# Kernel optimization log

Hardware: AMD Instinct MI355X
Metric: run time of the kernel (lower is better)

Reference implementation:

```python
import jax, jax.numpy as jnp
import numpy as np

B, N, K = 8, 12500, 64           # graphs, nodes/graph, sort-pool k
E_PER = 200000                   # edges per graph (avg degree 16)
TOTAL_N = B * N
TOTAL_E = B * E_PER
NEG_SLOPE = 0.01
EPS = 1e-5


def setup_inputs() -> dict:
    key = jax.random.key(0)
    ks = jax.random.split(key, 8)
    # per-graph local edge endpoints, then offset into the global node index space
    offs = (jnp.arange(B, dtype=jnp.int32) * N)[:, None]
    src = (jax.random.randint(ks[0], (B, E_PER), 0, N, dtype=jnp.int32) + offs).reshape(-1)
    dst = (jax.random.randint(ks[1], (B, E_PER), 0, N, dtype=jnp.int32) + offs).reshape(-1)
    return {
        "features": jax.random.normal(ks[2], (TOTAL_N, 64), dtype=jnp.float32),
        "edge_weights": jax.random.uniform(ks[3], (TOTAL_E,), dtype=jnp.float32),
        "W1": jax.random.normal(ks[4], (64, 128), dtype=jnp.float32) * (1.0 / np.sqrt(64)),
        "W2": jax.random.normal(ks[5], (128, 32), dtype=jnp.float32) * (1.0 / np.sqrt(128)),
        "gamma1": jnp.ones((128,), jnp.float32),
        "beta1": jnp.zeros((128,), jnp.float32),
        "alpha1": jnp.ones((128,), jnp.float32),
        "gamma2": jnp.ones((32,), jnp.float32),
        "beta2": jnp.zeros((32,), jnp.float32),
        "alpha2": jnp.ones((32,), jnp.float32),
        "edge_src": src,
        "edge_dst": dst,
    }


def _leaky(x):
    return jnp.where(x >= 0, x, NEG_SLOPE * x)


def _graph_conv(feat, W, src, dst, ew):
    # DGL GraphConv, norm='both', bias=False, with edge_weight.
    ones = jnp.ones((TOTAL_E,), feat.dtype)
    out_deg = jnp.maximum(jax.ops.segment_sum(ones, src, num_segments=TOTAL_N), 1.0)
    in_deg = jnp.maximum(jax.ops.segment_sum(ones, dst, num_segments=TOTAL_N), 1.0)
    h = (feat * jax.lax.rsqrt(out_deg)[:, None]) @ W          # project (linear, order-invariant)
    msg = h[src] * ew[:, None]                                 # [E, out]
    agg = jax.ops.segment_sum(msg, dst, num_segments=TOTAL_N)  # SpMM scatter
    return agg * jax.lax.rsqrt(in_deg)[:, None]


def _graph_norm(feat, gamma, beta, alpha):
    # per-graph GraphNorm: (x - alpha*mean) / sqrt(var(x - alpha*mean) + eps) * gamma + beta
    x = feat.reshape(B, N, -1)
    mean = x.mean(axis=1, keepdims=True)
    sub = x - alpha * mean
    var = (sub * sub).mean(axis=1, keepdims=True)
    out = gamma * sub * jax.lax.rsqrt(var + EPS) + beta
    return out.reshape(TOTAL_N, -1)


def _sort_pool(feat):
    # DGL SortPooling: sort each node's features ascending, take top-K nodes by last channel.
    x = jnp.sort(feat.reshape(B, N, -1), axis=-1)
    _, idx = jax.lax.top_k(x[..., -1], K)                      # [B, K], descending
    sel = jnp.take_along_axis(x, idx[..., None], axis=1)       # [B, K, D]
    return sel.reshape(B, -1)


def reference(features, edge_weights, W1, W2, gamma1, beta1, alpha1,
              gamma2, beta2, alpha2, edge_src, edge_dst):
    h1 = _graph_conv(features, W1, edge_src, edge_dst, edge_weights)
    h1 = _leaky(_graph_norm(h1, gamma1, beta1, alpha1))
    r1 = _sort_pool(h1)                                        # [B, K*128]
    h2 = _graph_conv(h1, W2, edge_src, edge_dst, edge_weights)
    h2 = _leaky(_graph_norm(h2, gamma2, beta2, alpha2))
    r2 = _sort_pool(h2)                                        # [B, K*32]
    return _leaky(jnp.concatenate([r1, r2], axis=1))           # [B, K*(128+32)]
```

## Files before the change

### kernel.cpp

```cpp
#include <hip/hip_runtime.h>
#include <cstdint>

constexpr int B_       = 8;
constexpr int NPG_     = 12500;
constexpr int KSEL_    = 64;
constexpr int TOTAL_N_ = 100000;
constexpr int TOTAL_E_ = 1600000;
constexpr int EPG_     = 200000;
constexpr int NKEY_    = 16384;
constexpr int OUT_ROW  = KSEL_ * (128 + 32);
constexpr int NB_SCAN  = (TOTAL_N_ + 255) / 256;
constexpr int BPG_     = (EPG_ + 255) / 256;

constexpr int TROWS_   = 32;
constexpr int NT_DST   = 391;
constexpr int NT_SRC   = 4;
constexpr int SRC_TW   = 3125;
constexpr int LBKT_    = NT_DST * 8 * NT_SRC;
constexpr int NBKT     = B_ * LBKT_;
constexpr int NB_BSCAN = NBKT / 256;

constexpr int BLKG_    = 16;
constexpr int NHB_     = B_ * BLKG_;
constexpr int ESLICE_  = EPG_ / BLKG_;

typedef float f2v __attribute__((ext_vector_type(2)));
typedef int   i2v __attribute__((ext_vector_type(2)));

__device__ __forceinline__ float lrelu(float v){ return v >= 0.f ? v : 0.01f * v; }
__device__ __forceinline__ int   rlanei(int x, int l){ return __builtin_amdgcn_readlane(x, l); }
__device__ __forceinline__ float rlanef(float x, int l){
  return __uint_as_float(__builtin_amdgcn_readlane((int)__float_as_uint(x), l));
}

__device__ __forceinline__ void edge_key(int s, int d, int& key, int& pk){
  int g   = d / NPG_;
  int dlc = d - g * NPG_;
  int slc = s - g * NPG_;
  int dt  = dlc >> 5;
  int dl  = dlc & 31;
  int w   = dl >> 2;
  int st  = slc / SRC_TW;
  key = (((g * NT_DST + dt) * 8 + w) * NT_SRC) + st;
  pk  = (slc << 2) | (dl & 3);
}

__global__ __launch_bounds__(1024, 1)
void hist_priv(const int* __restrict__ src, const int* __restrict__ dst,
               int* __restrict__ out_part,
               int* __restrict__ bkt_part,
               unsigned short* __restrict__ lrank){
  __shared__ int oh[NPG_];
  __shared__ int bh[LBKT_];
  int t  = threadIdx.x;
  int hb = blockIdx.x;
  int g  = hb & 7, sb = hb >> 3;
  for (int i = t; i < NPG_;  i += 1024) oh[i] = 0;
  for (int i = t; i < LBKT_; i += 1024) bh[i] = 0;
  __syncthreads();
  int ebase = g * EPG_ + sb * ESLICE_;
  for (int i = t; i < ESLICE_; i += 1024){
    int e = ebase + i;
    int s = src[e], d = dst[e];
    atomicAdd(&oh[s - g * NPG_], 1);
    int key, pk; edge_key(s, d, key, pk);
    int r = atomicAdd(&bh[key - g * LBKT_], 1);
    lrank[e] = (unsigned short)r;
  }
  __syncthreads();
  int* op = out_part + (size_t)hb * NPG_;
  int* bp = bkt_part + (size_t)hb * LBKT_;
  for (int i = t; i < NPG_;  i += 1024) op[i] = oh[i];
  for (int i = t; i < LBKT_; i += 1024) bp[i] = bh[i];
}

__global__ void hist_reduce_nodes(const int* __restrict__ out_part, float* __restrict__ rsq_out){
  int i = blockIdx.x * 256 + threadIdx.x;
  if (i < TOTAL_N_){
    int g = i / NPG_, nl = i - g * NPG_;
    int s = 0;
    #pragma unroll
    for (int sb = 0; sb < BLKG_; ++sb) s += out_part[(size_t)(sb * 8 + g) * NPG_ + nl];
    if (s < 1) s = 1;
    rsq_out[i] = rsqrtf((float)s);
  }
}

__global__ void hist_reduce_bkt(int* __restrict__ bkt_part, int* __restrict__ bcnt){
  int k = blockIdx.x * 256 + threadIdx.x;
  if (k < NBKT){
    int g = k / LBKT_, lk = k - g * LBKT_;
    int run = 0;
    #pragma unroll
    for (int sb = 0; sb < BLKG_; ++sb){
      size_t idx = (size_t)(sb * 8 + g) * LBKT_ + lk;
      int v = bkt_part[idx];
      bkt_part[idx] = run;
      run += v;
    }
    bcnt[k] = run;
  }
}

__global__ void scan_blocks(const int* __restrict__ cnt, int* __restrict__ off,
                            int* __restrict__ bsum, int n){
  __shared__ int tmp[256];
  int t = threadIdx.x;
  int i = blockIdx.x * 256 + t;
  int x = (i < n) ? cnt[i] : 0;
  tmp[t] = x;
  __syncthreads();
  for (int d = 1; d < 256; d <<= 1){
    int v = (t >= d) ? tmp[t - d] : 0;
    __syncthreads();
    tmp[t] += v;
    __syncthreads();
  }
  if (i < n) off[i] = tmp[t] - x;
  if (t == 255) bsum[blockIdx.x] = tmp[255];
}

__global__ void scan_sums(int* __restrict__ bsum, int nb){
  __shared__ int tmp[512];
  int t = threadIdx.x;
  int x = (t < nb) ? bsum[t] : 0;
  tmp[t] = x;
  __syncthreads();
  for (int d = 1; d < 512; d <<= 1){
    int v = (t >= d) ? tmp[t - d] : 0;
    __syncthreads();
    tmp[t] += v;
    __syncthreads();
  }
  if (t < nb) bsum[t] = tmp[t] - x;
}

__global__ void scan_add(int* __restrict__ off, const int* __restrict__ bsum, int n){
  int i = blockIdx.x * 256 + threadIdx.x;
  if (i < n) off[i] += bsum[blockIdx.x];
}

__global__ void bfill2(const int* __restrict__ src, const int* __restrict__ dst,
                       const float* __restrict__ ew, const float* __restrict__ rsq_out,
                       const unsigned short* __restrict__ lrank,
                       const int* __restrict__ bkt_part, const int* __restrict__ boff,
                       i2v* __restrict__ bkt){
  int g  = blockIdx.x & 7;
  int il = (blockIdx.x >> 3) * 256 + threadIdx.x;
  if (il < EPG_){
    int e = g * EPG_ + il;
    int s = src[e], d = dst[e];
    int key, pk; edge_key(s, d, key, pk);
    int lk = key - g * LBKT_;
    int sb = il / ESLICE_;
    int slot = boff[key] + bkt_part[(size_t)(sb * 8 + g) * LBKT_ + lk] + (int)lrank[e];
    i2v v; v.x = pk; v.y = __float_as_int(ew[e] * rsq_out[s]);
    bkt[slot] = v;
  }
}

__global__ __launch_bounds__(512, 4)
void spmm1_tile(const int* __restrict__ boff, const i2v* __restrict__ bkt,
                const float* __restrict__ feat, const float* __restrict__ W1,
                float* __restrict__ rsq_in, float* __restrict__ h1,
                float* __restrict__ gsum, float* __restrict__ gsq){
  __shared__ float wsh[64 * 128];
  __shared__ float sred[4][512];
  int t = threadIdx.x;
  int w = t >> 6, lane = t & 63;
  int g = blockIdx.x & 7, dt = blockIdx.x >> 3;

  for (int i = t; i < 64 * 128; i += 512) wsh[i] = W1[i];

  int kbase = (((g * NT_DST + dt) * 8) + w) * NT_SRC;
  int e0 = boff[kbase];
  int e1 = (kbase + NT_SRC < NBKT) ? boff[kbase + NT_SRC] : TOTAL_E_;

  const float* fg = feat + (size_t)g * NPG_ * 64;
  float a0 = 0.f, a1 = 0.f, a2 = 0.f, a3 = 0.f;
  int cntp = 0;

#define ACC1(P, Q, F) { int r_ = (P) & 3; float q_ = (Q);                 \
    a0 = fmaf((r_ == 0) ? q_ : 0.f, (F), a0);                             \
    a1 = fmaf((r_ == 1) ? q_ : 0.f, (F), a1);                             \
    a2 = fmaf((r_ == 2) ? q_ : 0.f, (F), a2);                             \
    a3 = fmaf((r_ == 3) ? q_ : 0.f, (F), a3);                             \
    cntp += 1 << (r_ << 3); }

  #pragma unroll 1
  for (int e = e0; e < e1; e += 64){
    int m = e1 - e; if (m > 64) m = 64;
    int pk = 0; float wr = 0.f;
    if (lane < m){ i2v ed = bkt[e + lane]; pk = ed.x; wr = __int_as_float(ed.y); }
    int j = 0;
    #pragma unroll 1
    for (; j + 8 <= m; j += 8){
      int   p0 = rlanei(pk, j+0), p1 = rlanei(pk, j+1), p2 = rlanei(pk, j+2), p3 = rlanei(pk, j+3);
      int   p4 = rlanei(pk, j+4), p5 = rlanei(pk, j+5), p6 = rlanei(pk, j+6), p7 = rlanei(pk, j+7);
      float q0 = rlanef(wr, j+0), q1 = rlanef(wr, j+1), q2 = rlanef(wr, j+2), q3 = rlanef(wr, j+3);
      float q4 = rlanef(wr, j+4), q5 = rlanef(wr, j+5), q6 = rlanef(wr, j+6), q7 = rlanef(wr, j+7);
      float f0 = fg[(size_t)(p0 >> 2) * 64 + lane];
      float f1 = fg[(size_t)(p1 >> 2) * 64 + lane];
      float f2 = fg[(size_t)(p2 >> 2) * 64 + lane];
      float f3 = fg[(size_t)(p3 >> 2) * 64 + lane];
      float f4 = fg[(size_t)(p4 >> 2) * 64 + lane];
      float f5 = fg[(size_t)(p5 >> 2) * 64 + lane];
      float f6 = fg[(size_t)(p6 >> 2) * 64 + lane];
      float f7 = fg[(size_t)(p7 >> 2) * 64 + lane];
      ACC1(p0, q0, f0); ACC1(p1, q1, f1); ACC1(p2, q2, f2); ACC1(p3, q3, f3);
      ACC1(p4, q4, f4); ACC1(p5, q5, f5); ACC1(p6, q6, f6); ACC1(p7, q7, f7);
    }
    #pragma unroll 1
    for (; j < m; ++j){
      int   p = rlanei(pk, j);
      float q = rlanef(wr, j);
      float f = fg[(size_t)(p >> 2) * 64 + lane];
      ACC1(p, q, f);
    }
  }
#undef ACC1

  __syncthreads();

  int rows = NPG_ - dt * TROWS_; if (rows > TROWS_) rows = TROWS_;
  const f2v* wp = (const f2v*)wsh;
  f2v A0 = {0.f,0.f}, A1 = {0.f,0.f}, A2 = {0.f,0.f}, A3 = {0.f,0.f};
  #pragma unroll 1
  for (int k = 0; k < 64; ++k){
    f2v wv = wp[k * 64 + lane];
    float b0 = rlanef(a0, k), b1 = rlanef(a1, k), b2 = rlanef(a2, k), b3 = rlanef(a3, k);
    A0.x = fmaf(b0, wv.x, A0.x); A0.y = fmaf(b0, wv.y, A0.y);
    A1.x = fmaf(b1, wv.x, A1.x); A1.y = fmaf(b1, wv.y, A1.y);
    A2.x = fmaf(b2, wv.x, A2.x); A2.y = fmaf(b2, wv.y, A2.y);
    A3.x = fmaf(b3, wv.x, A3.x); A3.y = fmaf(b3, wv.y, A3.y);
  }
  float s0 = 0.f, q0 = 0.f, s1 = 0.f, q1 = 0.f;
  #pragma unroll
  for (int r = 0; r < 4; ++r){
    int lr = w * 4 + r;
    if (lr < rows){
      f2v A = (r == 0) ? A0 : (r == 1) ? A1 : (r == 2) ? A2 : A3;
      int cr = (cntp >> (r << 3)) & 255;
      float ri = rsqrtf((float)(cr < 1 ? 1 : cr));
      int node = g * NPG_ + dt * TROWS_ + lr;
      if (lane == 0) rsq_in[node] = ri;
      A.x *= ri; A.y *= ri;
      __builtin_nontemporal_store(A, (f2v*)&h1[(size_t)node * 128 + 2 * lane]);
      s0 += A.x; q0 = fmaf(A.x, A.x, q0);
      s1 += A.y; q1 = fmaf(A.y, A.y, q1);
    }
  }
  __syncthreads();
  sred[0][t] = s0; sred[1][t] = q0; sred[2][t] = s1; sred[3][t] = q1;
  __syncthreads();
  if (t < 64){
    float S0 = 0.f, Q0 = 0.f, S1 = 0.f, Q1 = 0.f;
    #pragma unroll
    for (int ww = 0; ww < 8; ++ww){
      S0 += sred[0][t + 64*ww]; Q0 += sred[1][t + 64*ww];
      S1 += sred[2][t + 64*ww]; Q1 += sred[3][t + 64*ww];
    }
    atomicAdd(&gsum[g * 128 + 2*t],     S0);
    atomicAdd(&gsq [g * 128 + 2*t],     Q0);
    atomicAdd(&gsum[g * 128 + 2*t + 1], S1);
    atomicAdd(&gsq [g * 128 + 2*t + 1], Q1);
  }
}

__global__ void finalize1(const float* __restrict__ gsum, const float* __restrict__ gsq,
                          const float* __restrict__ gamma, const float* __restrict__ beta,
                          const float* __restrict__ alpha, float* __restrict__ mul, float* __restrict__ add){
  int i = threadIdx.x;
  int c = i & 127;
  const float invn = 1.0f / (float)NPG_;
  float m = gsum[i] * invn;
  float a = alpha[c];
  float var = gsq[i] * invn - 2.f * a * m * m + a * a * m * m;
  float mu = gamma[c] * rsqrtf(var + 1e-5f);
  mul[i] = mu;
  add[i] = beta[c] - mu * a * m;
}

__global__ __launch_bounds__(256, 4)
void normproj(const float* __restrict__ h1,
              const float* __restrict__ mul, const float* __restrict__ add,
              const float* __restrict__ W2,
              unsigned long long* __restrict__ keys, float* __restrict__ h2p){
  __shared__ float w2s[128 * 32];
  int t = threadIdx.x;
  for (int i = t; i < 128 * 32; i += 256) w2s[i] = W2[i];
  __syncthreads();

  int g     = blockIdx.x & 7;
  int wslot = (blockIdx.x >> 3) * 4 + (t >> 6);
  int lane  = t & 63;
  int c     = lane & 31, hh = lane >> 5;
  int wbase = hh * 64 * 32 + c;

  float m0 = mul[g * 128 + lane],      aa0 = add[g * 128 + lane];
  float m1 = mul[g * 128 + 64 + lane], aa1 = add[g * 128 + 64 + lane];

  int nv = (NPG_ - wslot + 511) / 512;

  int v0 = g * NPG_ + wslot;
  float x0 = __builtin_nontemporal_load(&h1[(size_t)v0 * 128 + lane]);
  float x1 = __builtin_nontemporal_load(&h1[(size_t)v0 * 128 + 64 + lane]);

  for (int i = 0; i < nv; ++i){
    int v = g * NPG_ + wslot + i * 512;
    float cur0 = x0, cur1 = x1;
    if (i + 1 < nv){
      int vn = v + 512;
      x0 = __builtin_nontemporal_load(&h1[(size_t)vn * 128 + lane]);
      x1 = __builtin_nontemporal_load(&h1[(size_t)vn * 128 + 64 + lane]);
    }
    float y0 = lrelu(fmaf(m0, cur0, aa0));
    float y1 = lrelu(fmaf(m1, cur1, aa1));
    float mx = fmaxf(y0, y1);
    for (int o = 1; o < 64; o <<= 1) mx = fmaxf(mx, __shfl_xor(mx, o));
    if (lane == 0){
      unsigned u = __float_as_uint(mx);
      u ^= (u >> 31) ? 0xFFFFFFFFu : 0x80000000u;
      int nloc = v - g * NPG_;
      keys[(size_t)g * NKEY_ + nloc] = ((unsigned long long)(~u) << 32) | (unsigned)nloc;
    }
    float acc = 0.f;
    #pragma unroll
    for (int kk = 0; kk < 64; ++kk){
      float sa = rlanef(y0, kk);
      float sb = rlanef(y1, kk);
      float vk = hh ? sb : sa;
      acc = fmaf(vk, w2s[wbase + kk * 32], acc);
    }
    acc += __shfl_xor(acc, 32);
    if (hh == 0) h2p[(size_t)v * 32 + c] = acc;
  }
}

__global__ void topk_s1(const unsigned long long* __restrict__ keys, unsigned long long* __restrict__ cand){
  __shared__ unsigned long long s[2048];
  int b = blockIdx.x >> 3, ch = blockIdx.x & 7;
  int t = threadIdx.x;
  for (int i = t; i < 2048; i += 256) s[i] = keys[(size_t)b * NKEY_ + (size_t)ch * 2048 + i];
  for (int k2 = 2; k2 <= 2048; k2 <<= 1){
    for (int j = k2 >> 1; j > 0; j >>= 1){
      __syncthreads();
      for (int i = t; i < 2048; i += 256){
        int p = i ^ j;
        if (p > i){
          unsigned long long A = s[i], C = s[p];
          bool up = ((i & k2) == 0);
          if ((A > C) == up){ s[i] = C; s[p] = A; }
        }
      }
    }
  }
  __syncthreads();
  if (t < 64) cand[(size_t)b * 512 + (size_t)ch * 64 + t] = s[t];
}

__global__ void topk_s2(const unsigned long long* __restrict__ cand, int* __restrict__ topidx){
  __shared__ unsigned long long s[512];
  int b = blockIdx.x;
  int t = threadIdx.x;
  for (int i = t; i < 512; i += 256) s[i] = cand[(size_t)b * 512 + i];
  for (int k2 = 2; k2 <= 512; k2 <<= 1){
    for (int j = k2 >> 1; j > 0; j >>= 1){
      __syncthreads();
      for (int i = t; i < 512; i += 256){
        int p = i ^ j;
        if (p > i){
          unsigned long long A = s[i], C = s[p];
          bool up = ((i & k2) == 0);
          if ((A > C) == up){ s[i] = C; s[p] = A; }
        }
      }
    }
  }
  __syncthreads();
  if (t < 64) topidx[b * 64 + t] = (int)(s[t] & 0xFFFFFFFFull);
}

__global__ void emit1(const float* __restrict__ h1, const int* __restrict__ topidx,
                      const float* __restrict__ mul, const float* __restrict__ add,
                      float* __restrict__ out){
  __shared__ float s[128];
  int b = blockIdx.x >> 6, k = blockIdx.x & 63;
  int t = threadIdx.x;
  int nloc = topidx[b * 64 + k];
  float raw = h1[((size_t)b * NPG_ + nloc) * 128 + t];
  s[t] = lrelu(fmaf(mul[b * 128 + t], raw, add[b * 128 + t]));
  for (int k2 = 2; k2 <= 128; k2 <<= 1){
    for (int j = k2 >> 1; j > 0; j >>= 1){
      __syncthreads();
      int p = t ^ j;
      if (p > t){
        float A = s[t], C = s[p];
        bool up = ((t & k2) == 0);
        if ((A > C) == up){ s[t] = C; s[p] = A; }
      }
    }
  }
  __syncthreads();
  out[(size_t)b * OUT_ROW + (size_t)k * 128 + t] = lrelu(s[t]);
}

__global__ __launch_bounds__(512, 4)
void spmm2_tile(const int* __restrict__ boff, const i2v* __restrict__ bkt,
                const float* __restrict__ h2p, const float* __restrict__ rsq_in,
                float* __restrict__ h2c, float* __restrict__ gsum, float* __restrict__ gsq){
  __shared__ float sred[2][512];
  int t = threadIdx.x;
  int w = t >> 6, lane = t & 63;
  int c = lane & 31, h = lane >> 5;
  int g = blockIdx.x & 7, dt = blockIdx.x >> 3;

  int kbase = (((g * NT_DST + dt) * 8) + w) * NT_SRC;
  int e0 = boff[kbase];
  int e1 = (kbase + NT_SRC < NBKT) ? boff[kbase + NT_SRC] : TOTAL_E_;

  const float* hg = h2p + (size_t)g * NPG_ * 32;
  float b0 = 0.f, b1 = 0.f;

#define ACC2(P, Q, F) { int r_ = (P) & 3;                                  \
    float wm_ = ((r_ & 1) == h) ? (Q) : 0.f;                               \
    if (r_ < 2) b0 = fmaf(wm_, (F), b0); else b1 = fmaf(wm_, (F), b1); }

  #pragma unroll 1
  for (int e = e0; e < e1; e += 64){
    int m = e1 - e; if (m > 64) m = 64;
    int pk = 0; float wr = 0.f;
    if (lane < m){ i2v ed = bkt[e + lane]; pk = ed.x; wr = __int_as_float(ed.y); }
    int j = 0;
    #pragma unroll 1
    for (; j + 4 <= m; j += 4){
      int   p0 = rlanei(pk, j+0), p1 = rlanei(pk, j+1), p2 = rlanei(pk, j+2), p3 = rlanei(pk, j+3);
      float q0 = rlanef(wr, j+0), q1 = rlanef(wr, j+1), q2 = rlanef(wr, j+2), q3 = rlanef(wr, j+3);
      float f0 = hg[(size_t)(p0 >> 2) * 32 + c];
      float f1 = hg[(size_t)(p1 >> 2) * 32 + c];
      float f2 = hg[(size_t)(p2 >> 2) * 32 + c];
      float f3 = hg[(size_t)(p3 >> 2) * 32 + c];
      ACC2(p0, q0, f0); ACC2(p1, q1, f1); ACC2(p2, q2, f2); ACC2(p3, q3, f3);
    }
    #pragma unroll 1
    for (; j < m; ++j){
      int   p = rlanei(pk, j);
      float q = rlanef(wr, j);
      float f = hg[(size_t)(p >> 2) * 32 + c];
      ACC2(p, q, f);
    }
  }
#undef ACC2

  int rows = NPG_ - dt * TROWS_; if (rows > TROWS_) rows = TROWS_;
  float ssum = 0.f, ssq = 0.f;
  {
    int l0 = w * 4 + h;
    if (l0 < rows){
      int node = g * NPG_ + dt * TROWS_ + l0;
      float val = b0 * rsq_in[node];
      __builtin_nontemporal_store(val, &h2c[(size_t)node * 32 + c]);
      ssum += val; ssq = fmaf(val, val, ssq);
    }
    int l1 = w * 4 + 2 + h;
    if (l1 < rows){
      int node = g * NPG_ + dt * TROWS_ + l1;
      float val = b1 * rsq_in[node];
      __builtin_nontemporal_store(val, &h2c[(size_t)node * 32 + c]);
      ssum += val; ssq = fmaf(val, val, ssq);
    }
  }
  __syncthreads();
  sred[0][t] = ssum; sred[1][t] = ssq;
  __syncthreads();
  if (t < 32){
    float S = 0.f, Q = 0.f;
    #pragma unroll
    for (int k = 0; k < 16; ++k){
      S += sred[0][t + 32 * k];
      Q += sred[1][t + 32 * k];
    }
    atomicAdd(&gsum[g * 32 + t], S);
    atomicAdd(&gsq [g * 32 + t], Q);
  }
}

__global__ void finalize2(const float* __restrict__ gsum, const float* __restrict__ gsq,
                          const float* __restrict__ gamma, const float* __restrict__ beta,
                          const float* __restrict__ alpha, float* __restrict__ mul, float* __restrict__ add){
  int i = threadIdx.x;
  int c = i & 31;
  const float invn = 1.0f / (float)NPG_;
  float m = gsum[i] * invn;
  float a = alpha[c];
  float var = gsq[i] * invn - 2.f * a * m * m + a * a * m * m;
  float mu = gamma[c] * rsqrtf(var + 1e-5f);
  mul[i] = mu;
  add[i] = beta[c] - mu * a * m;
}

__global__ void norm2(float* __restrict__ h, const float* __restrict__ mul, const float* __restrict__ add,
                      unsigned long long* __restrict__ keys){
  int tid  = blockIdx.x * 256 + threadIdx.x;
  int node = tid >> 5;
  int sl   = tid & 31;
  if (node >= TOTAL_N_) return;
  int b = node / NPG_;
  int nloc = node - b * NPG_;
  float v = h[(size_t)node * 32 + sl];
  v = lrelu(fmaf(mul[b * 32 + sl], v, add[b * 32 + sl]));
  h[(size_t)node * 32 + sl] = v;
  float m = v;
  for (int o = 1; o < 32; o <<= 1) m = fmaxf(m, __shfl_xor(m, o));
  if (sl == 0){
    unsigned u = __float_as_uint(m);
    u ^= (u >> 31) ? 0xFFFFFFFFu : 0x80000000u;
    keys[(size_t)b * NKEY_ + nloc] = ((unsigned long long)(~u) << 32) | (unsigned)nloc;
  }
}

__global__ void emit2(const float* __restrict__ h2, const int* __restrict__ topidx, float* __restrict__ out){
  int b = blockIdx.x >> 6, k = blockIdx.x & 63;
  int lane = threadIdx.x;
  int nloc = topidx[b * 64 + k];
  float v = h2[((size_t)b * NPG_ + nloc) * 32 + lane];
  for (int k2 = 2; k2 <= 32; k2 <<= 1){
    for (int j = k2 >> 1; j > 0; j >>= 1){
      float o = __shfl_xor(v, j);
      bool up    = ((lane & k2) == 0);
      bool lower = ((lane & j) == 0);
      v = (up == lower) ? fminf(v, o) : fmaxf(v, o);
    }
  }
  out[(size_t)b * OUT_ROW + 8192 + (size_t)k * 32 + lane] = lrelu(v);
}

__global__ void sentinel_kernel(float* out){
  int i = blockIdx.x * 256 + threadIdx.x;
  if (i < B_ * OUT_ROW) out[i] = -777.0f;
}

extern "C" void kernel_launch(void* const* d_in, const int* in_sizes, int n_in,
                              void* d_out, int out_size, void* d_ws, size_t ws_size,
                              hipStream_t stream){
  const float* feat   = (const float*)d_in[0];
  const float* ew     = (const float*)d_in[1];
  const float* W1     = (const float*)d_in[2];
  const float* W2     = (const float*)d_in[3];
  const float* gamma1 = (const float*)d_in[4];
  const float* beta1  = (const float*)d_in[5];
  const float* alpha1 = (const float*)d_in[6];
  const float* gamma2 = (const float*)d_in[7];
  const float* beta2  = (const float*)d_in[8];
  const float* alpha2 = (const float*)d_in[9];
  const int*   esrc   = (const int*)d_in[10];
  const int*   edst   = (const int*)d_in[11];
  float* out = (float*)d_out;

  char* ws = (char*)d_ws;
  auto alloc = [&](size_t bytes) -> char* {
    char* p = ws;
    ws += (bytes + 255) & ~(size_t)255;
    return p;
  };

  float* gsum1   = (float*)alloc(1024 * 4);
  float* gsq1    = (float*)alloc(1024 * 4);
  float* gsum2   = (float*)alloc(256 * 4);
  float* gsq2    = (float*)alloc(256 * 4);
  size_t zero_bytes = (size_t)(ws - (char*)d_ws);

  float* rsq_in  = (float*)alloc((size_t)TOTAL_N_ * 4);
  float* rsq_out = (float*)alloc((size_t)TOTAL_N_ * 4);
  int*   out_part= (int*)  alloc((size_t)NHB_ * NPG_ * 4);
  int*   bkt_part= (int*)  alloc((size_t)NHB_ * LBKT_ * 4);
  unsigned short* lrank = (unsigned short*)alloc((size_t)TOTAL_E_ * 2);
  int*   bcnt    = (int*)  alloc((size_t)NBKT * 4);
  int*   boff    = (int*)  alloc((size_t)NBKT * 4);
  int*   bsum    = (int*)  alloc(512 * 4);
  float* mul1    = (float*)alloc(1024 * 4);
  float* add1    = (float*)alloc(1024 * 4);
  float* mul2    = (float*)alloc(256 * 4);
  float* add2    = (float*)alloc(256 * 4);
  int*   topidx1 = (int*)  alloc(512 * 4);
  int*   topidx2 = (int*)  alloc(512 * 4);
  unsigned long long* cand = (unsigned long long*)alloc((size_t)B_ * 512 * 8);
  unsigned long long* keys = (unsigned long long*)alloc((size_t)B_ * NKEY_ * 8);
  i2v*   bkt     = (i2v*)  alloc((size_t)TOTAL_E_ * 8);
  float* h2p     = (float*)alloc((size_t)TOTAL_N_ * 32 * 4);
  float* h2c     = (float*)alloc((size_t)TOTAL_N_ * 32 * 4);
  float* h1      = (float*)alloc((size_t)TOTAL_N_ * 128 * 4);

  size_t need = (size_t)(ws - (char*)d_ws);
  if (need > ws_size){
    sentinel_kernel<<<(B_ * OUT_ROW + 255) / 256, 256, 0, stream>>>(out);
    return;
  }

  hipMemsetAsync(d_ws, 0, zero_bytes, stream);
  hipMemsetAsync(keys, 0xFF, (size_t)B_ * NKEY_ * 8, stream);

  hist_priv        <<<NHB_, 1024, 0, stream>>>(esrc, edst, out_part, bkt_part, lrank);
  hist_reduce_nodes<<<NB_SCAN, 256, 0, stream>>>(out_part, rsq_out);
  hist_reduce_bkt  <<<NB_BSCAN, 256, 0, stream>>>(bkt_part, bcnt);
  scan_blocks      <<<NB_BSCAN, 256, 0, stream>>>(bcnt, boff, bsum, NBKT);
  scan_sums        <<<1, 512, 0, stream>>>(bsum, NB_BSCAN);
  scan_add         <<<NB_BSCAN, 256, 0, stream>>>(boff, bsum, NBKT);
  bfill2           <<<8 * BPG_, 256, 0, stream>>>(esrc, edst, ew, rsq_out, lrank,
                                                  bkt_part, boff, bkt);

  spmm1_tile <<<NT_DST * 8, 512, 0, stream>>>(boff, bkt, feat, W1, rsq_in, h1, gsum1, gsq1);
  finalize1  <<<1, 1024, 0, stream>>>(gsum1, gsq1, gamma1, beta1, alpha1, mul1, add1);
  normproj   <<<1024, 256, 0, stream>>>(h1, mul1, add1, W2, keys, h2p);
  topk_s1    <<<B_ * 8, 256, 0, stream>>>(keys, cand);
  topk_s2    <<<B_, 256, 0, stream>>>(cand, topidx1);
  emit1      <<<B_ * 64, 128, 0, stream>>>(h1, topidx1, mul1, add1, out);

  spmm2_tile <<<NT_DST * 8, 512, 0, stream>>>(boff, bkt, h2p, rsq_in, h2c, gsum2, gsq2);
  finalize2  <<<1, 256, 0, stream>>>(gsum2, gsq2, gamma2, beta2, alpha2, mul2, add2);
  norm2      <<<TOTAL_N_ * 32 / 256, 256, 0, stream>>>(h2c, mul2, add2, keys);
  topk_s1    <<<B_ * 8, 256, 0, stream>>>(keys, cand);
  topk_s2    <<<B_, 256, 0, stream>>>(cand, topidx2);
  emit2      <<<B_ * 64, 32, 0, stream>>>(h2c, topidx2, out);
}
```

Measured before the change: 459.2 us.

## Bucket edges per destination row to drop masked four-way accumulation in SpMM

Edge buckets are now keyed by individual destination row (32 rows × 2 source tiles) rather than by group of four rows × 4 source tiles. Each warp can then process one row's segment at a time with plain FMAs instead of four masked FMAs per edge. In-degree comes from the segment length, so the rsq_in array is no longer needed. This doubles the bucket count, so the histogram uses two shared arrays and the scan runs with 1024 threads. It also adds per-row loop overhead and shorter segments, which lowers gather batching.

```diff
diff --git a/kernel.cpp b/kernel.cpp
--- a/kernel.cpp
+++ b/kernel.cpp
@@ -14,9 +14,10 @@
 
 constexpr int TROWS_   = 32;
 constexpr int NT_DST   = 391;
-constexpr int NT_SRC   = 4;
-constexpr int SRC_TW   = 3125;
-constexpr int LBKT_    = NT_DST * 8 * NT_SRC;
+constexpr int NT_SRC   = 2;
+constexpr int SRC_TW   = 6250;
+constexpr int LBKT_    = NT_DST * 8 * 4 * NT_SRC;
+constexpr int LBH_     = LBKT_ / 2;
 constexpr int NBKT     = B_ * LBKT_;
 constexpr int NB_BSCAN = NBKT / 256;
 
@@ -39,10 +40,9 @@
   int slc = s - g * NPG_;
   int dt  = dlc >> 5;
   int dl  = dlc & 31;
-  int w   = dl >> 2;
   int st  = slc / SRC_TW;
-  key = (((g * NT_DST + dt) * 8 + w) * NT_SRC) + st;
-  pk  = (slc << 2) | (dl & 3);
+  key = ((g * NT_DST + dt) * 32 + dl) * NT_SRC + st;
+  pk  = slc;
 }
 
 __global__ __launch_bounds__(1024, 1)
@@ -50,13 +50,14 @@
                int* __restrict__ out_part,
                int* __restrict__ bkt_part,
                unsigned short* __restrict__ lrank){
-  __shared__ int oh[NPG_];
-  __shared__ int bh[LBKT_];
+  __shared__ int oh [NPG_];
+  __shared__ int bhA[LBH_];
+  __shared__ int bhB[LBH_];
   int t  = threadIdx.x;
   int hb = blockIdx.x;
   int g  = hb & 7, sb = hb >> 3;
-  for (int i = t; i < NPG_;  i += 1024) oh[i] = 0;
-  for (int i = t; i < LBKT_; i += 1024) bh[i] = 0;
+  for (int i = t; i < NPG_; i += 1024) oh[i] = 0;
+  for (int i = t; i < LBH_; i += 1024){ bhA[i] = 0; bhB[i] = 0; }
   __syncthreads();
   int ebase = g * EPG_ + sb * ESLICE_;
   for (int i = t; i < ESLICE_; i += 1024){
@@ -64,14 +65,15 @@
     int s = src[e], d = dst[e];
     atomicAdd(&oh[s - g * NPG_], 1);
     int key, pk; edge_key(s, d, key, pk);
-    int r = atomicAdd(&bh[key - g * LBKT_], 1);
+    int lk = key - g * LBKT_;
+    int r = (lk < LBH_) ? atomicAdd(&bhA[lk], 1) : atomicAdd(&bhB[lk - LBH_], 1);
     lrank[e] = (unsigned short)r;
   }
   __syncthreads();
   int* op = out_part + (size_t)hb * NPG_;
   int* bp = bkt_part + (size_t)hb * LBKT_;
-  for (int i = t; i < NPG_;  i += 1024) op[i] = oh[i];
-  for (int i = t; i < LBKT_; i += 1024) bp[i] = bh[i];
+  for (int i = t; i < NPG_; i += 1024) op[i] = oh[i];
+  for (int i = t; i < LBH_; i += 1024){ bp[i] = bhA[i]; bp[LBH_ + i] = bhB[i]; }
 }
 
 __global__ void hist_reduce_nodes(const int* __restrict__ out_part, float* __restrict__ rsq_out){
@@ -121,12 +123,12 @@
 }
 
 __global__ void scan_sums(int* __restrict__ bsum, int nb){
-  __shared__ int tmp[512];
+  __shared__ int tmp[1024];
   int t = threadIdx.x;
   int x = (t < nb) ? bsum[t] : 0;
   tmp[t] = x;
   __syncthreads();
-  for (int d = 1; d < 512; d <<= 1){
+  for (int d = 1; d < 1024; d <<= 1){
     int v = (t >= d) ? tmp[t - d] : 0;
     __syncthreads();
     tmp[t] += v;
@@ -162,8 +164,7 @@
 __global__ __launch_bounds__(512, 4)
 void spmm1_tile(const int* __restrict__ boff, const i2v* __restrict__ bkt,
                 const float* __restrict__ feat, const float* __restrict__ W1,
-                float* __restrict__ rsq_in, float* __restrict__ h1,
-                float* __restrict__ gsum, float* __restrict__ gsq){
+                float* __restrict__ h1, float* __restrict__ gsum, float* __restrict__ gsq){
   __shared__ float wsh[64 * 128];
   __shared__ float sred[4][512];
   int t = threadIdx.x;
@@ -172,53 +173,50 @@
 
   for (int i = t; i < 64 * 128; i += 512) wsh[i] = W1[i];
 
-  int kbase = (((g * NT_DST + dt) * 8) + w) * NT_SRC;
-  int e0 = boff[kbase];
-  int e1 = (kbase + NT_SRC < NBKT) ? boff[kbase + NT_SRC] : TOTAL_E_;
-
+  int wk = ((g * NT_DST + dt) * 32 + w * 4) * NT_SRC;
   const float* fg = feat + (size_t)g * NPG_ * 64;
-  float a0 = 0.f, a1 = 0.f, a2 = 0.f, a3 = 0.f;
-  int cntp = 0;
-
-#define ACC1(P, Q, F) { int r_ = (P) & 3; float q_ = (Q);                 \
-    a0 = fmaf((r_ == 0) ? q_ : 0.f, (F), a0);                             \
-    a1 = fmaf((r_ == 1) ? q_ : 0.f, (F), a1);                             \
-    a2 = fmaf((r_ == 2) ? q_ : 0.f, (F), a2);                             \
-    a3 = fmaf((r_ == 3) ? q_ : 0.f, (F), a3);                             \
-    cntp += 1 << (r_ << 3); }
-
-  #pragma unroll 1
-  for (int e = e0; e < e1; e += 64){
-    int m = e1 - e; if (m > 64) m = 64;
-    int pk = 0; float wr = 0.f;
-    if (lane < m){ i2v ed = bkt[e + lane]; pk = ed.x; wr = __int_as_float(ed.y); }
-    int j = 0;
-    #pragma unroll 1
-    for (; j + 8 <= m; j += 8){
-      int   p0 = rlanei(pk, j+0), p1 = rlanei(pk, j+1), p2 = rlanei(pk, j+2), p3 = rlanei(pk, j+3);
-      int   p4 = rlanei(pk, j+4), p5 = rlanei(pk, j+5), p6 = rlanei(pk, j+6), p7 = rlanei(pk, j+7);
-      float q0 = rlanef(wr, j+0), q1 = rlanef(wr, j+1), q2 = rlanef(wr, j+2), q3 = rlanef(wr, j+3);
-      float q4 = rlanef(wr, j+4), q5 = rlanef(wr, j+5), q6 = rlanef(wr, j+6), q7 = rlanef(wr, j+7);
-      float f0 = fg[(size_t)(p0 >> 2) * 64 + lane];
-      float f1 = fg[(size_t)(p1 >> 2) * 64 + lane];
-      float f2 = fg[(size_t)(p2 >> 2) * 64 + lane];
-      float f3 = fg[(size_t)(p3 >> 2) * 64 + lane];
-      float f4 = fg[(size_t)(p4 >> 2) * 64 + lane];
-      float f5 = fg[(size_t)(p5 >> 2) * 64 + lane];
-      float f6 = fg[(size_t)(p6 >> 2) * 64 + lane];
-      float f7 = fg[(size_t)(p7 >> 2) * 64 + lane];
-      ACC1(p0, q0, f0); ACC1(p1, q1, f1); ACC1(p2, q2, f2); ACC1(p3, q3, f3);
-      ACC1(p4, q4, f4); ACC1(p5, q5, f5); ACC1(p6, q6, f6); ACC1(p7, q7, f7);
-    }
-    #pragma unroll 1
-    for (; j < m; ++j){
-      int   p = rlanei(pk, j);
-      float q = rlanef(wr, j);
-      float f = fg[(size_t)(p >> 2) * 64 + lane];
-      ACC1(p, q, f);
-    }
-  }
-#undef ACC1
+
+  float a0, a1, a2, a3;
+  int   c0, c1, c2, c3;
+
+#define SEG1(R, ACC, CR) {                                                   \
+    int i1v = wk + (R + 1) * NT_SRC;                                         \
+    int se0 = boff[wk + R * NT_SRC];                                         \
+    int se1 = (i1v < NBKT) ? boff[i1v] : TOTAL_E_;                           \
+    CR = se1 - se0;                                                          \
+    float accA = 0.f, accB = 0.f;                                            \
+    for (int e = se0; e < se1; e += 64){                                     \
+      int m = se1 - e; if (m > 64) m = 64;                                   \
+      int pk = 0; float wr = 0.f;                                            \
+      if (lane < m){ i2v ed = bkt[e + lane]; pk = ed.x; wr = __int_as_float(ed.y); } \
+      int j = 0;                                                             \
+      for (; j + 8 <= m; j += 8){                                            \
+        int   p0 = rlanei(pk, j+0), p1 = rlanei(pk, j+1), p2 = rlanei(pk, j+2), p3 = rlanei(pk, j+3); \
+        int   p4 = rlanei(pk, j+4), p5 = rlanei(pk, j+5), p6 = rlanei(pk, j+6), p7 = rlanei(pk, j+7); \
+        float q0 = rlanef(wr, j+0), q1 = rlanef(wr, j+1), q2 = rlanef(wr, j+2), q3 = rlanef(wr, j+3); \
+        float q4 = rlanef(wr, j+4), q5 = rlanef(wr, j+5), q6 = rlanef(wr, j+6), q7 = rlanef(wr, j+7); \
+        float f0 = fg[(size_t)p0 * 64 + lane];                               \
+        float f1 = fg[(size_t)p1 * 64 + lane];                               \
+        float f2 = fg[(size_t)p2 * 64 + lane];                               \
+        float f3 = fg[(size_t)p3 * 64 + lane];                               \
+        float f4 = fg[(size_t)p4 * 64 + lane];                               \
+        float f5 = fg[(size_t)p5 * 64 + lane];                               \
+        float f6 = fg[(size_t)p6 * 64 + lane];                               \
+        float f7 = fg[(size_t)p7 * 64 + lane];                               \
+        accA = fmaf(q0, f0, accA); accB = fmaf(q1, f1, accB);                \
+        accA = fmaf(q2, f2, accA); accB = fmaf(q3, f3, accB);                \
+        accA = fmaf(q4, f4, accA); accB = fmaf(q5, f5, accB);                \
+        accA = fmaf(q6, f6, accA); accB = fmaf(q7, f7, accB);                \
+      }                                                                      \
+      for (; j < m; ++j){                                                    \
+        int p = rlanei(pk, j); float q = rlanef(wr, j);                      \
+        accA = fmaf(q, fg[(size_t)p * 64 + lane], accA);                     \
+      }                                                                      \
+    }                                                                        \
+    ACC = accA + accB; }
+
+  SEG1(0, a0, c0); SEG1(1, a1, c1); SEG1(2, a2, c2); SEG1(3, a3, c3);
+#undef SEG1
 
   __syncthreads();
 
@@ -240,10 +238,9 @@
     int lr = w * 4 + r;
     if (lr < rows){
       f2v A = (r == 0) ? A0 : (r == 1) ? A1 : (r == 2) ? A2 : A3;
-      int cr = (cntp >> (r << 3)) & 255;
+      int cr = (r == 0) ? c0 : (r == 1) ? c1 : (r == 2) ? c2 : c3;
       float ri = rsqrtf((float)(cr < 1 ? 1 : cr));
       int node = g * NPG_ + dt * TROWS_ + lr;
-      if (lane == 0) rsq_in[node] = ri;
       A.x *= ri; A.y *= ri;
       __builtin_nontemporal_store(A, (f2v*)&h1[(size_t)node * 128 + 2 * lane]);
       s0 += A.x; q0 = fmaf(A.x, A.x, q0);
@@ -407,69 +404,66 @@
 
 __global__ __launch_bounds__(512, 4)
 void spmm2_tile(const int* __restrict__ boff, const i2v* __restrict__ bkt,
-                const float* __restrict__ h2p, const float* __restrict__ rsq_in,
-                float* __restrict__ h2c, float* __restrict__ gsum, float* __restrict__ gsq){
+                const float* __restrict__ h2p, float* __restrict__ h2c,
+                float* __restrict__ gsum, float* __restrict__ gsq){
   __shared__ float sred[2][512];
   int t = threadIdx.x;
   int w = t >> 6, lane = t & 63;
   int c = lane & 31, h = lane >> 5;
   int g = blockIdx.x & 7, dt = blockIdx.x >> 3;
 
-  int kbase = (((g * NT_DST + dt) * 8) + w) * NT_SRC;
-  int e0 = boff[kbase];
-  int e1 = (kbase + NT_SRC < NBKT) ? boff[kbase + NT_SRC] : TOTAL_E_;
-
+  int wk = ((g * NT_DST + dt) * 32 + w * 4) * NT_SRC;
   const float* hg = h2p + (size_t)g * NPG_ * 32;
-  float b0 = 0.f, b1 = 0.f;
-
-#define ACC2(P, Q, F) { int r_ = (P) & 3;                                  \
-    float wm_ = ((r_ & 1) == h) ? (Q) : 0.f;                               \
-    if (r_ < 2) b0 = fmaf(wm_, (F), b0); else b1 = fmaf(wm_, (F), b1); }
-
-  #pragma unroll 1
-  for (int e = e0; e < e1; e += 64){
-    int m = e1 - e; if (m > 64) m = 64;
-    int pk = 0; float wr = 0.f;
-    if (lane < m){ i2v ed = bkt[e + lane]; pk = ed.x; wr = __int_as_float(ed.y); }
-    int j = 0;
-    #pragma unroll 1
-    for (; j + 4 <= m; j += 4){
-      int   p0 = rlanei(pk, j+0), p1 = rlanei(pk, j+1), p2 = rlanei(pk, j+2), p3 = rlanei(pk, j+3);
-      float q0 = rlanef(wr, j+0), q1 = rlanef(wr, j+1), q2 = rlanef(wr, j+2), q3 = rlanef(wr, j+3);
-      float f0 = hg[(size_t)(p0 >> 2) * 32 + c];
-      float f1 = hg[(size_t)(p1 >> 2) * 32 + c];
-      float f2 = hg[(size_t)(p2 >> 2) * 32 + c];
-      float f3 = hg[(size_t)(p3 >> 2) * 32 + c];
-      ACC2(p0, q0, f0); ACC2(p1, q1, f1); ACC2(p2, q2, f2); ACC2(p3, q3, f3);
-    }
-    #pragma unroll 1
-    for (; j < m; ++j){
-      int   p = rlanei(pk, j);
-      float q = rlanef(wr, j);
-      float f = hg[(size_t)(p >> 2) * 32 + c];
-      ACC2(p, q, f);
-    }
-  }
-#undef ACC2
-
   int rows = NPG_ - dt * TROWS_; if (rows > TROWS_) rows = TROWS_;
+
   float ssum = 0.f, ssq = 0.f;
-  {
-    int l0 = w * 4 + h;
-    if (l0 < rows){
-      int node = g * NPG_ + dt * TROWS_ + l0;
-      float val = b0 * rsq_in[node];
+
+  #pragma unroll
+  for (int r = 0; r < 4; ++r){
+    int i1v = wk + (r + 1) * NT_SRC;
+    int se0 = boff[wk + r * NT_SRC];
+    int se1 = (i1v < NBKT) ? boff[i1v] : TOTAL_E_;
+    int cr  = se1 - se0;
+    float acc = 0.f;
+    for (int e = se0; e < se1; e += 64){
+      int m = se1 - e; if (m > 64) m = 64;
+      int pk = 0; float wr = 0.f;
+      if (lane < m){ i2v ed = bkt[e + lane]; pk = ed.x; wr = __int_as_float(ed.y); }
+      int j = 0;
+      for (; j + 4 <= m; j += 4){
+        int   pA0 = rlanei(pk, j+0), pB0 = rlanei(pk, j+1);
+        int   pA1 = rlanei(pk, j+2), pB1 = rlanei(pk, j+3);
+        float qA0 = rlanef(wr, j+0), qB0 = rlanef(wr, j+1);
+        float qA1 = rlanef(wr, j+2), qB1 = rlanef(wr, j+3);
+        int   p0 = h ? pB0 : pA0;  float q0 = h ? qB0 : qA0;
+        int   p1 = h ? pB1 : pA1;  float q1 = h ? qB1 : qA1;
+        float f0 = hg[(size_t)p0 * 32 + c];
+        float f1 = hg[(size_t)p1 * 32 + c];
+        acc = fmaf(q0, f0, acc); acc = fmaf(q1, f1, acc);
+      }
+      for (; j + 2 <= m; j += 2){
+        int   pA = rlanei(pk, j), pB = rlanei(pk, j+1);
+        float qA = rlanef(wr, j), qB = rlanef(wr, j+1);
+        int   p = h ? pB : pA;  float q = h ? qB : qA;
+        acc = fmaf(q, hg[(size_t)p * 32 + c], acc);
+      }
+      if (j < m){
+        int   p = rlanei(pk, j);
+        float q = h ? 0.f : rlanef(wr, j);
+        acc = fmaf(q, hg[(size_t)p * 32 + c], acc);
+      }
+    }
+    acc += __shfl_xor(acc, 32);
+    int lr = w * 4 + r;
+    if (lr < rows && h == 0){
+      float ri = rsqrtf((float)(cr < 1 ? 1 : cr));
+      float val = acc * ri;
+      int node = g * NPG_ + dt * TROWS_ + lr;
       __builtin_nontemporal_store(val, &h2c[(size_t)node * 32 + c]);
       ssum += val; ssq = fmaf(val, val, ssq);
     }
-    int l1 = w * 4 + 2 + h;
-    if (l1 < rows){
-      int node = g * NPG_ + dt * TROWS_ + l1;
-      float val = b1 * rsq_in[node];
-      __builtin_nontemporal_store(val, &h2c[(size_t)node * 32 + c]);
-      ssum += val; ssq = fmaf(val, val, ssq);
-    }
-  }
+  }
+
   __syncthreads();
   sred[0][t] = ssum; sred[1][t] = ssq;
   __syncthreads();
@@ -570,14 +564,13 @@
   float* gsq2    = (float*)alloc(256 * 4);
   size_t zero_bytes = (size_t)(ws - (char*)d_ws);
 
-  float* rsq_in  = (float*)alloc((size_t)TOTAL_N_ * 4);
   float* rsq_out = (float*)alloc((size_t)TOTAL_N_ * 4);
   int*   out_part= (int*)  alloc((size_t)NHB_ * NPG_ * 4);
   int*   bkt_part= (int*)  alloc((size_t)NHB_ * LBKT_ * 4);
   unsigned short* lrank = (unsigned short*)alloc((size_t)TOTAL_E_ * 2);
   int*   bcnt    = (int*)  alloc((size_t)NBKT * 4);
   int*   boff    = (int*)  alloc((size_t)NBKT * 4);
-  int*   bsum    = (int*)  alloc(512 * 4);
+  int*   bsum    = (int*)  alloc(1024 * 4);
   float* mul1    = (float*)alloc(1024 * 4);
   float* add1    = (float*)alloc(1024 * 4);
   float* mul2    = (float*)alloc(256 * 4);
@@ -604,19 +597,19 @@
   hist_reduce_nodes<<<NB_SCAN, 256, 0, stream>>>(out_part, rsq_out);
   hist_reduce_bkt  <<<NB_BSCAN, 256, 0, stream>>>(bkt_part, bcnt);
   scan_blocks      <<<NB_BSCAN, 256, 0, stream>>>(bcnt, boff, bsum, NBKT);
-  scan_sums        <<<1, 512, 0, stream>>>(bsum, NB_BSCAN);
+  scan_sums        <<<1, 1024, 0, stream>>>(bsum, NB_BSCAN);
   scan_add         <<<NB_BSCAN, 256, 0, stream>>>(boff, bsum, NBKT);
   bfill2           <<<8 * BPG_, 256, 0, stream>>>(esrc, edst, ew, rsq_out, lrank,
                                                   bkt_part, boff, bkt);
 
-  spmm1_tile <<<NT_DST * 8, 512, 0, stream>>>(boff, bkt, feat, W1, rsq_in, h1, gsum1, gsq1);
+  spmm1_tile <<<NT_DST * 8, 512, 0, stream>>>(boff, bkt, feat, W1, h1, gsum1, gsq1);
   finalize1  <<<1, 1024, 0, stream>>>(gsum1, gsq1, gamma1, beta1, alpha1, mul1, add1);
   normproj   <<<1024, 256, 0, stream>>>(h1, mul1, add1, W2, keys, h2p);
   topk_s1    <<<B_ * 8, 256, 0, stream>>>(keys, cand);
   topk_s2    <<<B_, 256, 0, stream>>>(cand, topidx1);
   emit1      <<<B_ * 64, 128, 0, stream>>>(h1, topidx1, mul1, add1, out);
 
-  spmm2_tile <<<NT_DST * 8, 512, 0, stream>>>(boff, bkt, h2p, rsq_in, h2c, gsum2, gsq2);
+  spmm2_tile <<<NT_DST * 8, 512, 0, stream>>>(boff, bkt, h2p, h2c, gsum2, gsq2);
   finalize2  <<<1, 256, 0, stream>>>(gsum2, gsq2, gamma2, beta2, alpha2, mul2, add2);
   norm2      <<<TOTAL_N_ * 32 / 256, 256, 0, stream>>>(h2c, mul2, add2, keys);
   topk_s1    <<<B_ * 8, 256, 0, stream>>>(keys, cand);
```

After: 446.1 us. -2.8%, faster.
